# Performance work log

Hardware: AMD Instinct MI355X
Metric: run time of the kernel (lower is better)

## Reference

```python
import jax, jax.numpy as jnp
import numpy as np

D_MODEL = 1024
D_STATE = 16
D_CONV = 3
D_INNER = 2 * D_MODEL  # expand=2
B, S = 4, 2048


def setup_inputs() -> dict:
    key = jax.random.key(0)
    ks = jax.random.split(key, 9)
    s = 0.02
    x = jax.random.normal(ks[0], (B, S, D_MODEL), jnp.float32)
    # Linear weights stored as [in, out] so y = x @ W (equivalent to torch x @ W.T)
    in_proj_w = jax.random.normal(ks[1], (D_MODEL, 2 * D_INNER), jnp.float32) * s
    conv_w = jax.random.normal(ks[2], (D_INNER, 1, D_CONV), jnp.float32) * s  # depthwise, OIW
    conv_b = jax.random.normal(ks[3], (D_INNER,), jnp.float32) * s
    x_proj_w = jax.random.normal(ks[4], (D_INNER, D_INNER + 2 * D_STATE), jnp.float32) * s
    dt_proj_w = jax.random.normal(ks[5], (D_INNER, D_INNER), jnp.float32) * s
    dt_proj_b = jax.random.normal(ks[6], (D_INNER,), jnp.float32) * s
    out_proj_w = jax.random.normal(ks[7], (D_INNER, D_MODEL), jnp.float32) * s
    A_log = jnp.tile(jnp.log(jnp.arange(1, D_STATE + 1, dtype=jnp.float32))[None, :], (D_INNER, 1))
    D_param = jnp.ones((D_INNER,), jnp.float32)
    return {"x": x, "in_proj_w": in_proj_w, "conv_w": conv_w, "conv_b": conv_b,
            "x_proj_w": x_proj_w, "dt_proj_w": dt_proj_w, "dt_proj_b": dt_proj_b,
            "out_proj_w": out_proj_w, "A_log": A_log, "D_param": D_param}


def _mamba_forward(x, in_proj_w, conv_w, conv_b, x_proj_w, dt_proj_w, dt_proj_b,
                   out_proj_w, A_log, D_param):
    combined = x @ in_proj_w                      # [B,S,2*d_inner]
    u, x_gate = jnp.split(combined, 2, axis=-1)
    # depthwise 1D conv, SAME padding (padding = d_conv//2)
    u_c = jax.lax.conv_general_dilated(
        u.transpose(0, 2, 1), conv_w, window_strides=(1,), padding='SAME',
        feature_group_count=D_INNER, dimension_numbers=('NCW', 'OIW', 'NCW'))
    u = jax.nn.silu((u_c + conv_b[None, :, None]).transpose(0, 2, 1))  # [B,S,d_inner]
    x_dbl = u @ x_proj_w
    delta, b, c = jnp.split(x_dbl, [D_INNER, D_INNER + D_STATE], axis=-1)
    delta = jax.nn.softplus(delta @ dt_proj_w + dt_proj_b)             # [B,S,d_inner]
    a = -jnp.exp(A_log)                                                # [d_inner,d_state]

    def step(h, inp):
        u_t, d_t, b_t, c_t = inp                 # [B,d_inner], [B,d_inner], [B,d_state], [B,d_state]
        h = jnp.exp(d_t[:, :, None] * a) * h + (d_t[:, :, None] * b_t[:, None, :]) * u_t[:, :, None]
        y_t = jnp.einsum('bds,bs->bd', h, c_t)
        return h, y_t

    h0 = jnp.zeros((x.shape[0], D_INNER, D_STATE), x.dtype)
    xs = (u.transpose(1, 0, 2), delta.transpose(1, 0, 2),
          b.transpose(1, 0, 2), c.transpose(1, 0, 2))
    _, ys = jax.lax.scan(step, h0, xs)           # ys: [S,B,d_inner]
    y = ys.transpose(1, 0, 2)
    y = y + u * D_param
    y = y * jax.nn.silu(x_gate)
    return y @ out_proj_w                        # [B,S,d_model]


def reference(x, in_proj_w, conv_w, conv_b, x_proj_w, dt_proj_w, dt_proj_b,
              out_proj_w, A_log, D_param):
    return _mamba_forward(x, in_proj_w, conv_w, conv_b, x_proj_w, dt_proj_w,
                          dt_proj_b, out_proj_w, A_log, D_param)
```

## Files before the change

### kernel.cpp

```cpp
#include <hip/hip_runtime.h>
#include <hip/hip_bf16.h>
#include <cstddef>
#include <cstdint>


typedef __hip_bfloat16 bf16;
typedef unsigned int u32;
typedef short short8 __attribute__((ext_vector_type(8)));
typedef float f32x4 __attribute__((ext_vector_type(4)));

#define GLOBAL_AS __attribute__((address_space(1)))
#define LDS_AS    __attribute__((address_space(3)))

__device__ __forceinline__ float bf2f(short s) {
    union { float f; u32 u; } x; x.u = ((u32)(unsigned short)s) << 16; return x.f;
}
__device__ __forceinline__ void store_c(float* p, float v) { *p = v; }
__device__ __forceinline__ void store_c(bf16* p, float v)  { *p = __float2bfloat16(v); }

__device__ __forceinline__ int xcd_swizzle(int orig, int nwg) {
    return ((nwg & 7) == 0) ? ((orig & 7) * (nwg >> 3) + (orig >> 3)) : orig;
}

#define BAR()   do { __builtin_amdgcn_s_barrier(); asm volatile("" ::: "memory"); } while (0)
#define VMW4()  asm volatile("s_waitcnt vmcnt(4)" ::: "memory")
#define VMW0()  asm volatile("s_waitcnt vmcnt(0)" ::: "memory")

__global__ __launch_bounds__(512, 2) void gemm256(
    const bf16* __restrict__ A, const bf16* __restrict__ Bt,
    bf16* __restrict__ C, int N, int K, int lda, int ldb, int ldc)
{
    __shared__ short As[3][256 * 32];
    __shared__ short Bs[3][256 * 32];

    const int tid  = threadIdx.x;
    const int lane = tid & 63;
    const int wid  = tid >> 6;
    const int wr   = wid >> 2;
    const int wc   = wid & 3;

    const int gx   = gridDim.x;
    const int wgid = xcd_swizzle(blockIdx.y * gx + blockIdx.x, gx * gridDim.y);
    const int m0   = (wgid / gx) * 256;
    const int n0   = (wgid % gx) * 256;

    const int st_ks = (((tid & 3) ^ ((tid >> 3) & 3)) << 3);
    const int st_r  = tid >> 2;

    const int l15   = lane & 15;
    const int slotp = (((lane >> 4) ^ ((l15 >> 1) & 3)) << 3);

    f32x4 acc[8][4] = {};

    const int KT = K >> 5;

    auto STAGE2 = [&](int sl, int kti, int pr) {
        const int kbase = kti << 5;
        #pragma unroll
        for (int q = 0; q < 2; ++q) {
            int lrow = q * 128 + st_r;
            if (pr == 0) {
                const bf16* g = A + (size_t)(m0 + lrow) * lda + kbase + st_ks;
                __builtin_amdgcn_global_load_lds((const GLOBAL_AS u32*)g,
                    (LDS_AS u32*)(&As[sl][q * 4096 + tid * 8]), 16, 0, 0);
            } else {
                const bf16* g = Bt + (size_t)(n0 + lrow) * ldb + kbase + st_ks;
                __builtin_amdgcn_global_load_lds((const GLOBAL_AS u32*)g,
                    (LDS_AS u32*)(&Bs[sl][q * 4096 + tid * 8]), 16, 0, 0);
            }
        }
    };

    STAGE2(0, 0, 0); STAGE2(0, 0, 1);
    STAGE2(1, 1, 0); STAGE2(1, 1, 1);
    VMW4(); BAR();

    int sl = 0;
    #pragma unroll 1
    for (int kt = 0; kt < KT; ++kt) {
        const bool ds = (kt + 2 < KT);
        const int ns = (sl == 0) ? 2 : sl - 1;
        short8 a[4], b[4];

        #pragma unroll
        for (int j = 0; j < 4; ++j) {
            int row = wc * 64 + j * 16 + l15;
            b[j] = *(const short8*)&Bs[sl][row * 32 + slotp];
        }
        #pragma unroll
        for (int i = 0; i < 4; ++i) {
            int row = wr * 128 + i * 16 + l15;
            a[i] = *(const short8*)&As[sl][row * 32 + slotp];
        }
        if (ds) STAGE2(ns, kt + 2, 0);
        BAR();
        __builtin_amdgcn_s_setprio(1);
        #pragma unroll
        for (int i = 0; i < 4; ++i)
            #pragma unroll
            for (int j = 0; j < 4; ++j)
                acc[i][j] = __builtin_amdgcn_mfma_f32_16x16x32_bf16(
                    a[i], b[j], acc[i][j], 0, 0, 0);
        __builtin_amdgcn_s_setprio(0);
        BAR();

        #pragma unroll
        for (int i = 0; i < 4; ++i) {
            int row = wr * 128 + (4 + i) * 16 + l15;
            a[i] = *(const short8*)&As[sl][row * 32 + slotp];
        }
        if (ds) STAGE2(ns, kt + 2, 1);
        BAR();
        __builtin_amdgcn_s_setprio(1);
        #pragma unroll
        for (int i = 0; i < 4; ++i)
            #pragma unroll
            for (int j = 0; j < 4; ++j)
                acc[4 + i][j] = __builtin_amdgcn_mfma_f32_16x16x32_bf16(
                    a[i], b[j], acc[4 + i][j], 0, 0, 0);
        __builtin_amdgcn_s_setprio(0);
        if (ds) { VMW4(); } else { VMW0(); }
        BAR();
        sl = (sl == 2) ? 0 : sl + 1;
    }

    const int cl = lane & 15;
    const int rq = lane >> 4;
    #pragma unroll
    for (int i = 0; i < 8; ++i) {
        #pragma unroll
        for (int j = 0; j < 4; ++j) {
            int gc = n0 + wc * 64 + j * 16 + cl;
            if (gc >= N) continue;
            #pragma unroll
            for (int f = 0; f < 4; ++f) {
                int gr = m0 + wr * 128 + i * 16 + rq * 4 + f;
                C[(size_t)gr * ldc + gc] = __float2bfloat16(acc[i][j][f]);
            }
        }
    }
}

template <typename TC, bool ROT>
__global__ __launch_bounds__(256) void gemm_mfma(
    const bf16* __restrict__ A, const bf16* __restrict__ Bt,
    TC* __restrict__ C, int N, int K, int lda, int ldb, int ldc)
{
    __shared__ short As[128 * 64];
    __shared__ short Bs[128 * 64];

    const int tid  = threadIdx.x;
    const int lane = tid & 63;
    const int w    = tid >> 6;
    const int wr   = w >> 1, wc = w & 1;

    const int gx   = gridDim.x;
    const int wgid = xcd_swizzle(blockIdx.y * gx + blockIdx.x, gx * gridDim.y);
    const int m0   = (wgid / gx) * 128;
    const int n0   = (wgid % gx) * 128;

    const int lr = tid >> 3;
    const int s8 = tid & 7;

    f32x4 acc[4][4] = {};

    const int KT = K >> 6;
    for (int kt = 0; kt < KT; ++kt) {
        const int kte = ROT ? ((kt + wgid) & (KT - 1)) : kt;
        const int k0 = kte << 6;
        #pragma unroll
        for (int q = 0; q < 4; ++q) {
            int r = q * 32 + lr;
            int ks = (s8 ^ (r & 7)) * 8;
            const bf16* ga = A + (size_t)(m0 + r) * lda + k0 + ks;
            __builtin_amdgcn_global_load_lds((const GLOBAL_AS u32*)ga,
                (LDS_AS u32*)(As + q * 2048 + tid * 8), 16, 0, 0);
        }
        #pragma unroll
        for (int q = 0; q < 4; ++q) {
            int r = q * 32 + lr;
            int ks = (s8 ^ (r & 7)) * 8;
            const bf16* gb = Bt + (size_t)(n0 + r) * ldb + k0 + ks;
            __builtin_amdgcn_global_load_lds((const GLOBAL_AS u32*)gb,
                (LDS_AS u32*)(Bs + q * 2048 + tid * 8), 16, 0, 0);
        }
        __syncthreads();
        #pragma unroll
        for (int s = 0; s < 2; ++s) {
            short8 af[4], bfr[4];
            #pragma unroll
            for (int i = 0; i < 4; ++i) {
                int r = wr * 64 + i * 16 + (lane & 15);
                int slot = ((s << 2) + (lane >> 4)) ^ (r & 7);
                af[i] = *(const short8*)&As[r * 64 + slot * 8];
            }
            #pragma unroll
            for (int j = 0; j < 4; ++j) {
                int r = wc * 64 + j * 16 + (lane & 15);
                int slot = ((s << 2) + (lane >> 4)) ^ (r & 7);
                bfr[j] = *(const short8*)&Bs[r * 64 + slot * 8];
            }
            #pragma unroll
            for (int i = 0; i < 4; ++i)
                #pragma unroll
                for (int j = 0; j < 4; ++j)
                    acc[i][j] = __builtin_amdgcn_mfma_f32_16x16x32_bf16(
                        af[i], bfr[j], acc[i][j], 0, 0, 0);
        }
        __syncthreads();
    }

    const int cl = lane & 15;
    const int rq = lane >> 4;
    #pragma unroll
    for (int i = 0; i < 4; ++i) {
        #pragma unroll
        for (int j = 0; j < 4; ++j) {
            int gc = n0 + wc * 64 + j * 16 + cl;
            if (gc >= N) continue;
            #pragma unroll
            for (int f = 0; f < 4; ++f) {
                int gr = m0 + wr * 64 + i * 16 + rq * 4 + f;
                store_c(&C[(size_t)gr * ldc + gc], acc[i][j][f]);
            }
        }
    }
}

__global__ __launch_bounds__(256) void transpose_cast(
    const float* __restrict__ src, bf16* __restrict__ dst,
    int K, int Nsrc, int ldsrc, int Npad)
{
    __shared__ float t[32][33];
    int n0 = blockIdx.x * 32, k0 = blockIdx.y * 32;
    int lx = threadIdx.x & 31, ly = threadIdx.x >> 5;
    #pragma unroll
    for (int i = 0; i < 4; ++i) {
        int k = k0 + ly + 8 * i, n = n0 + lx;
        t[ly + 8 * i][lx] = (n < Nsrc) ? src[(size_t)k * ldsrc + n] : 0.f;
    }
    __syncthreads();
    #pragma unroll
    for (int i = 0; i < 4; ++i) {
        int n = n0 + ly + 8 * i;
        if (n < Npad) dst[(size_t)n * K + k0 + lx] = __float2bfloat16(t[lx][ly + 8 * i]);
    }
}

__global__ __launch_bounds__(256) void cast_x_kernel(
    const float* __restrict__ x, bf16* __restrict__ xb)
{
    int i = blockIdx.x * 256 + threadIdx.x;
    float4 v = ((const float4*)x)[i];
    alignas(8) bf16 h[4] = {__float2bfloat16(v.x), __float2bfloat16(v.y),
                            __float2bfloat16(v.z), __float2bfloat16(v.w)};
    ((ushort4*)xb)[i] = *(ushort4*)h;
}

__global__ __launch_bounds__(256) void conv_silu(
    const bf16* __restrict__ ur, const float* __restrict__ cw,
    const float* __restrict__ cb, bf16* __restrict__ uc)
{
    int idx = blockIdx.x * 256 + threadIdx.x;
    int d8 = idx & 255;
    int m  = idx >> 8;
    int s  = m & 2047;
    int d0 = d8 << 3;

    short8 z = {0, 0, 0, 0, 0, 0, 0, 0};
    short8 u0 = *(const short8*)&ur[(size_t)m * 2048 + d0];
    short8 um = (s > 0)    ? *(const short8*)&ur[(size_t)(m - 1) * 2048 + d0] : z;
    short8 up = (s < 2047) ? *(const short8*)&ur[(size_t)(m + 1) * 2048 + d0] : z;

    float wv[24];
    #pragma unroll
    for (int q = 0; q < 6; ++q) *(float4*)&wv[q * 4] = ((const float4*)(cw + d0 * 3))[q];
    float bv[8];
    *(float4*)&bv[0] = ((const float4*)(cb + d0))[0];
    *(float4*)&bv[4] = ((const float4*)(cb + d0))[1];

    alignas(16) bf16 o[8];
    #pragma unroll
    for (int i = 0; i < 8; ++i) {
        float acc = bv[i] + wv[i * 3] * bf2f(um[i]) + wv[i * 3 + 1] * bf2f(u0[i])
                  + wv[i * 3 + 2] * bf2f(up[i]);
        float sig = 1.f / (1.f + __expf(-acc));
        o[i] = __float2bfloat16(acc * sig);
    }
    *(short8*)&uc[(size_t)m * 2048 + d0] = *(short8*)o;
}

__global__ __launch_bounds__(256) void scan_partial(
    const bf16* __restrict__ draw,
    const bf16* __restrict__ uc,
    const bf16* __restrict__ bc,
    const float* __restrict__ dtb,
    float* __restrict__ hout, float* __restrict__ aprod)
{
    int d = blockIdx.x * 256 + threadIdx.x;
    int c = blockIdx.y;
    int b = blockIdx.z;

    float dtbv = dtb[d];
    float hl[16] = {};
    float E = 1.f;

    size_t mbase = (size_t)b * 2048 + c * 64;
    for (int s = 0; s < 64; ++s) {
        size_t m = mbase + s;
        float x  = bf2f(*(const short*)&draw[m * 2048 + d]) + dtbv;
        float t  = __expf(x);
        float t1 = 1.f + t;
        float e1 = 1.f / t1;
        float dv = __logf(t1);
        float uv = bf2f(*(const short*)&uc[m * 2048 + d]);
        const short8* bp = (const short8*)&bc[m * 32];
        short8 B0 = bp[0], B1 = bp[1];
        float du = dv * uv;
        float ep = e1;
        #pragma unroll
        for (int n = 0; n < 16; ++n) {
            float Bn = bf2f(n < 8 ? B0[n] : B1[n - 8]);
            hl[n] = ep * hl[n] + du * Bn;
            ep *= e1;
        }
        E *= e1;
    }
    float Pp = E;
    #pragma unroll
    for (int n = 0; n < 16; ++n) {
        int idx = (((b * 32 + c) * 16 + n) << 11) + d;
        hout[idx]  = hl[n];
        aprod[idx] = Pp;
        Pp *= E;
    }
}

__global__ __launch_bounds__(256) void scan_combine(
    float* hout, const float* __restrict__ aprod)
{
    int d = blockIdx.x * 256 + threadIdx.x;
    int n = blockIdx.y;
    int b = blockIdx.z;
    float H = 0.f;
    for (int c = 0; c < 32; ++c) {
        int idx = (((b * 32 + c) * 16 + n) << 11) + d;
        float he = hout[idx];
        float Pp = aprod[idx];
        hout[idx] = H;
        H = Pp * H + he;
    }
}

__global__ __launch_bounds__(256) void scan_final(
    const bf16* __restrict__ draw,
    const bf16* __restrict__ uc,
    const bf16* __restrict__ bc,
    const float* __restrict__ hin,
    const float* __restrict__ dtb,
    const float* __restrict__ D_param,
    bf16* ygate)
{
    int d = blockIdx.x * 256 + threadIdx.x;
    int c = blockIdx.y;
    int b = blockIdx.z;

    float h[16];
    #pragma unroll
    for (int n = 0; n < 16; ++n)
        h[n] = hin[(((b * 32 + c) * 16 + n) << 11) + d];
    float dtbv = dtb[d];
    float Dp = D_param[d];

    size_t mbase = (size_t)b * 2048 + c * 64;
    float xg_cur = bf2f(*(const short*)&ygate[mbase * 2048 + d]);

    for (int s = 0; s < 64; ++s) {
        size_t m = mbase + s;
        float x  = bf2f(*(const short*)&draw[m * 2048 + d]) + dtbv;
        float t  = __expf(x);
        float t1 = 1.f + t;
        float e1 = 1.f / t1;
        float dv = __logf(t1);
        float uv = bf2f(*(const short*)&uc[m * 2048 + d]);
        const short8* bp = (const short8*)&bc[m * 32];
        short8 B0 = bp[0], B1 = bp[1], C0 = bp[2], C1 = bp[3];
        float du = dv * uv;
        float ep = e1;
        float y = 0.f;
        #pragma unroll
        for (int n = 0; n < 16; ++n) {
            float Bn = bf2f(n < 8 ? B0[n] : B1[n - 8]);
            float Cn = bf2f(n < 8 ? C0[n] : C1[n - 8]);
            h[n] = ep * h[n] + du * Bn;
            y = fmaf(h[n], Cn, y);
            ep *= e1;
        }
        float xgv = xg_cur;
        if (s < 63) xg_cur = bf2f(*(const short*)&ygate[(m + 1) * 2048 + d]);
        float sig = 1.f / (1.f + __expf(-xgv));
        float y2 = (y + uv * Dp) * (xgv * sig);
        ygate[m * 2048 + d] = __float2bfloat16(y2);
    }
}

extern "C" void kernel_launch(void* const* d_in, const int* in_sizes, int n_in,
                              void* d_out, int out_size, void* d_ws, size_t ws_size,
                              hipStream_t stream) {
    const float* x    = (const float*)d_in[0];
    const float* w1   = (const float*)d_in[1];
    const float* cw   = (const float*)d_in[2];
    const float* cb   = (const float*)d_in[3];
    const float* w2   = (const float*)d_in[4];
    const float* w3   = (const float*)d_in[5];
    const float* dtb  = (const float*)d_in[6];
    const float* w4   = (const float*)d_in[7];
    const float* dpar = (const float*)d_in[9];
    float* out = (float*)d_out;

    const size_t MB = 1u << 20;
    const size_t needed = 152 * MB;
    if (ws_size < needed) return;

    char* p = (char*)d_ws;
    bf16*  xbf    = (bf16*)(p);
    bf16*  w1t    = (bf16*)(p + 16 * MB);
    bf16*  w2t    = (bf16*)(p);
    bf16*  w3t    = (bf16*)(p + 8912896);
    bf16*  w4t    = (bf16*)(p + 8912896 + 8388608);
    bf16*  bc     = (bf16*)(p + 8912896 + 8388608 + 4194304);
    bf16*  u_raw  = (bf16*)(p + 24 * MB);
    bf16*  draw   = u_raw;
    bf16*  uc     = (bf16*)(p + 56 * MB);
    bf16*  xg     = (bf16*)(p + 88 * MB);
    bf16*  xdblm  = (bf16*)(p + 120 * MB);
    float* summ_h = out;
    float* summ_a = out + (size_t)4 * 1024 * 1024;

    cast_x_kernel<<<8192, 256, 0, stream>>>(x, xbf);
    transpose_cast<<<dim3(128, 32), 256, 0, stream>>>(w1, w1t, 1024, 4096, 4096, 4096);

    gemm256<<<dim3(8, 32), 512, 0, stream>>>(
        xbf, w1t, u_raw, 2048, 1024, 1024, 1024, 2048);
    gemm256<<<dim3(8, 32), 512, 0, stream>>>(
        xbf, w1t + (size_t)2048 * 1024, xg, 2048, 1024, 1024, 1024, 2048);

    transpose_cast<<<dim3(68, 64), 256, 0, stream>>>(w2, w2t, 2048, 2080, 2080, 2176);
    transpose_cast<<<dim3(64, 64), 256, 0, stream>>>(w3, w3t, 2048, 2048, 2048, 2048);
    transpose_cast<<<dim3(32, 64), 256, 0, stream>>>(w4, w4t, 2048, 1024, 1024, 1024);

    conv_silu<<<8192, 256, 0, stream>>>(u_raw, cw, cb, uc);

    gemm256<<<dim3(8, 32), 512, 0, stream>>>(
        uc, w2t, xdblm, 2048, 2048, 2048, 2048, 2048);
    gemm_mfma<bf16, false><<<dim3(1, 64), 256, 0, stream>>>(
        uc, w2t + (size_t)2048 * 2048, bc, 32, 2048, 2048, 2048, 32);

    gemm256<<<dim3(8, 32), 512, 0, stream>>>(
        xdblm, w3t, draw, 2048, 2048, 2048, 2048, 2048);

    scan_partial<<<dim3(8, 32, 4), 256, 0, stream>>>(
        draw, uc, bc, dtb, summ_h, summ_a);
    scan_combine<<<dim3(8, 16, 4), 256, 0, stream>>>(summ_h, summ_a);
    scan_final<<<dim3(8, 32, 4), 256, 0, stream>>>(
        draw, uc, bc, summ_h, dtb, dpar, xg);

    gemm_mfma<float, true><<<dim3(8, 64), 256, 0, stream>>>(
        xg, w4t, out, 1024, 2048, 2048, 2048, 1024);
}
```

Before: 479.6 us.

## Deepen gemm256 LDS pipeline to four stages and keep B/C projections in fp32

Result: no change. 474.3 us (-1.1%).

```diff
diff --git a/kernel.cpp b/kernel.cpp
--- a/kernel.cpp
+++ b/kernel.cpp
@@ -23,6 +23,7 @@
 }
 
 #define BAR()   do { __builtin_amdgcn_s_barrier(); asm volatile("" ::: "memory"); } while (0)
+#define VMW8()  asm volatile("s_waitcnt vmcnt(8)" ::: "memory")
 #define VMW4()  asm volatile("s_waitcnt vmcnt(4)" ::: "memory")
 #define VMW0()  asm volatile("s_waitcnt vmcnt(0)" ::: "memory")
 
@@ -30,8 +31,8 @@
     const bf16* __restrict__ A, const bf16* __restrict__ Bt,
     bf16* __restrict__ C, int N, int K, int lda, int ldb, int ldc)
 {
-    __shared__ short As[3][256 * 32];
-    __shared__ short Bs[3][256 * 32];
+    __shared__ short As[4][256 * 32];
+    __shared__ short Bs[4][256 * 32];
 
     const int tid  = threadIdx.x;
     const int lane = tid & 63;
@@ -73,13 +74,14 @@
 
     STAGE2(0, 0, 0); STAGE2(0, 0, 1);
     STAGE2(1, 1, 0); STAGE2(1, 1, 1);
-    VMW4(); BAR();
+    STAGE2(2, 2, 0); STAGE2(2, 2, 1);
+    VMW8(); BAR();
 
     int sl = 0;
     #pragma unroll 1
     for (int kt = 0; kt < KT; ++kt) {
-        const bool ds = (kt + 2 < KT);
-        const int ns = (sl == 0) ? 2 : sl - 1;
+        const bool ds = (kt + 3 < KT);
+        const int ns = (sl + 3) & 3;
         short8 a[4], b[4];
 
         #pragma unroll
@@ -92,7 +94,7 @@
             int row = wr * 128 + i * 16 + l15;
             a[i] = *(const short8*)&As[sl][row * 32 + slotp];
         }
-        if (ds) STAGE2(ns, kt + 2, 0);
+        if (ds) STAGE2(ns, kt + 3, 0);
         BAR();
         __builtin_amdgcn_s_setprio(1);
         #pragma unroll
@@ -109,7 +111,7 @@
             int row = wr * 128 + (4 + i) * 16 + l15;
             a[i] = *(const short8*)&As[sl][row * 32 + slotp];
         }
-        if (ds) STAGE2(ns, kt + 2, 1);
+        if (ds) STAGE2(ns, kt + 3, 1);
         BAR();
         __builtin_amdgcn_s_setprio(1);
         #pragma unroll
@@ -119,9 +121,11 @@
                 acc[4 + i][j] = __builtin_amdgcn_mfma_f32_16x16x32_bf16(
                     a[i], b[j], acc[4 + i][j], 0, 0, 0);
         __builtin_amdgcn_s_setprio(0);
-        if (ds) { VMW4(); } else { VMW0(); }
+        if (kt + 3 < KT)      { VMW8(); }
+        else if (kt + 2 < KT) { VMW4(); }
+        else                  { VMW0(); }
         BAR();
-        sl = (sl == 2) ? 0 : sl + 1;
+        sl = (sl + 1) & 3;
     }
 
     const int cl = lane & 15;
@@ -293,7 +297,7 @@
 __global__ __launch_bounds__(256) void scan_partial(
     const bf16* __restrict__ draw,
     const bf16* __restrict__ uc,
-    const bf16* __restrict__ bc,
+    const float* __restrict__ bcf,
     const float* __restrict__ dtb,
     float* __restrict__ hout, float* __restrict__ aprod)
 {
@@ -314,14 +318,17 @@
         float e1 = 1.f / t1;
         float dv = __logf(t1);
         float uv = bf2f(*(const short*)&uc[m * 2048 + d]);
-        const short8* bp = (const short8*)&bc[m * 32];
-        short8 B0 = bp[0], B1 = bp[1];
+        const float4* bp = (const float4*)&bcf[m * 32];
+        float Bv[16];
+        *(float4*)&Bv[0]  = bp[0];
+        *(float4*)&Bv[4]  = bp[1];
+        *(float4*)&Bv[8]  = bp[2];
+        *(float4*)&Bv[12] = bp[3];
         float du = dv * uv;
         float ep = e1;
         #pragma unroll
         for (int n = 0; n < 16; ++n) {
-            float Bn = bf2f(n < 8 ? B0[n] : B1[n - 8]);
-            hl[n] = ep * hl[n] + du * Bn;
+            hl[n] = ep * hl[n] + du * Bv[n];
             ep *= e1;
         }
         E *= e1;
@@ -355,7 +362,7 @@
 __global__ __launch_bounds__(256) void scan_final(
     const bf16* __restrict__ draw,
     const bf16* __restrict__ uc,
-    const bf16* __restrict__ bc,
+    const float* __restrict__ bcf,
     const float* __restrict__ hin,
     const float* __restrict__ dtb,
     const float* __restrict__ D_param,
@@ -383,17 +390,23 @@
         float e1 = 1.f / t1;
         float dv = __logf(t1);
         float uv = bf2f(*(const short*)&uc[m * 2048 + d]);
-        const short8* bp = (const short8*)&bc[m * 32];
-        short8 B0 = bp[0], B1 = bp[1], C0 = bp[2], C1 = bp[3];
+        const float4* bp = (const float4*)&bcf[m * 32];
+        float Bv[16], Cv[16];
+        *(float4*)&Bv[0]  = bp[0];
+        *(float4*)&Bv[4]  = bp[1];
+        *(float4*)&Bv[8]  = bp[2];
+        *(float4*)&Bv[12] = bp[3];
+        *(float4*)&Cv[0]  = bp[4];
+        *(float4*)&Cv[4]  = bp[5];
+        *(float4*)&Cv[8]  = bp[6];
+        *(float4*)&Cv[12] = bp[7];
         float du = dv * uv;
         float ep = e1;
         float y = 0.f;
         #pragma unroll
         for (int n = 0; n < 16; ++n) {
-            float Bn = bf2f(n < 8 ? B0[n] : B1[n - 8]);
-            float Cn = bf2f(n < 8 ? C0[n] : C1[n - 8]);
-            h[n] = ep * h[n] + du * Bn;
-            y = fmaf(h[n], Cn, y);
+            h[n] = ep * h[n] + du * Bv[n];
+            y = fmaf(h[n], Cv[n], y);
             ep *= e1;
         }
         float xgv = xg_cur;
@@ -428,7 +441,7 @@
     bf16*  w2t    = (bf16*)(p);
     bf16*  w3t    = (bf16*)(p + 8912896);
     bf16*  w4t    = (bf16*)(p + 8912896 + 8388608);
-    bf16*  bc     = (bf16*)(p + 8912896 + 8388608 + 4194304);
+    float* bcf    = (float*)(p + 8912896 + 8388608 + 4194304);
     bf16*  u_raw  = (bf16*)(p + 24 * MB);
     bf16*  draw   = u_raw;
     bf16*  uc     = (bf16*)(p + 56 * MB);
@@ -453,17 +466,17 @@
 
     gemm256<<<dim3(8, 32), 512, 0, stream>>>(
         uc, w2t, xdblm, 2048, 2048, 2048, 2048, 2048);
-    gemm_mfma<bf16, false><<<dim3(1, 64), 256, 0, stream>>>(
-        uc, w2t + (size_t)2048 * 2048, bc, 32, 2048, 2048, 2048, 32);
+    gemm_mfma<float, false><<<dim3(1, 64), 256, 0, stream>>>(
+        uc, w2t + (size_t)2048 * 2048, bcf, 32, 2048, 2048, 2048, 32);
 
     gemm256<<<dim3(8, 32), 512, 0, stream>>>(
         xdblm, w3t, draw, 2048, 2048, 2048, 2048, 2048);
 
     scan_partial<<<dim3(8, 32, 4), 256, 0, stream>>>(
-        draw, uc, bc, dtb, summ_h, summ_a);
+        draw, uc, bcf, dtb, summ_h, summ_a);
     scan_combine<<<dim3(8, 16, 4), 256, 0, stream>>>(summ_h, summ_a);
     scan_final<<<dim3(8, 32, 4), 256, 0, stream>>>(
-        draw, uc, bc, summ_h, dtb, dpar, xg);
+        draw, uc, bcf, summ_h, dtb, dpar, xg);
 
     gemm_mfma<float, true><<<dim3(8, 64), 256, 0, stream>>>(
         xg, w4t, out, 1024, 2048, 2048, 2048, 1024);
```
